# Optimization experiments

Hardware: AMD Instinct MI355X
Metric: run time of the kernel (lower is better)

## Reference

```python
import jax, jax.numpy as jnp
import numpy as np

N_NODES = 100000
N_EDGES = 3200000
IN_DIM, HID1, HID2 = 128, 32, 16


def setup_inputs() -> dict:
    key = jax.random.key(0)
    ks = jax.random.split(key, 4)
    x = jax.random.normal(ks[0], (N_NODES, IN_DIM), dtype=jnp.float32)
    # glorot-ish scaling for weights
    W1 = jax.random.normal(ks[1], (IN_DIM, HID1), dtype=jnp.float32) * (1.0 / np.sqrt(IN_DIM))
    b1 = jnp.zeros((HID1,), dtype=jnp.float32)
    W2 = jax.random.normal(ks[2], (HID1, HID2), dtype=jnp.float32) * (1.0 / np.sqrt(HID1))
    b2 = jnp.zeros((HID2,), dtype=jnp.float32)
    edge_index = jax.random.randint(ks[3], (2, N_EDGES), 0, N_NODES, dtype=jnp.int64)
    return {"x": x, "W1": W1, "b1": b1, "W2": W2, "b2": b2, "edge_index": edge_index}


def _gcn_norm(edge_index, n_nodes):
    # add self loops, then symmetric normalization D^-1/2 (A+I) D^-1/2
    loops = jnp.arange(n_nodes, dtype=edge_index.dtype)
    src = jnp.concatenate([edge_index[0], loops])  # [E+N]
    dst = jnp.concatenate([edge_index[1], loops])
    deg = jax.ops.segment_sum(jnp.ones_like(dst, dtype=jnp.float32), dst, num_segments=n_nodes)
    inv_sqrt = jnp.where(deg > 0, jax.lax.rsqrt(jnp.maximum(deg, 1.0)), 0.0)
    norm = inv_sqrt[src] * inv_sqrt[dst]  # [E+N]
    return src, dst, norm


def _gcn_conv(x, W, b, src, dst, norm, n_nodes):
    xw = x @ W                                   # [N, out] transform first (out < in)
    msg = xw[src] * norm[:, None]                # gather + scale  [E+N, out]
    agg = jax.ops.segment_sum(msg, dst, num_segments=n_nodes)  # scatter-add
    return agg + b


def reference(x, W1, b1, W2, b2, edge_index):
    n = x.shape[0]
    src, dst, norm = _gcn_norm(edge_index, n)  # cached=True: same norm both layers
    h = _gcn_conv(x, W1, b1, src, dst, norm, n)
    h = jax.nn.relu(h)
    out = _gcn_conv(h, W2, b2, src, dst, norm, n)
    return out
```

## Files before the change

### kernel.cpp

```cpp
#include <hip/hip_runtime.h>


#define IN_DIM 128
#define HID1 32
#define HID2 16

#define BSHIFT 8
#define MAXNB 1024
#define SLABCAP 9216
#define P2_TILE 4096
#define P2_PER_THREAD 16

__device__ __forceinline__ float4 f4add(float4 a, float4 b) {
    a.x += b.x; a.y += b.y; a.z += b.z; a.w += b.w; return a;
}

__device__ __forceinline__ void load_edge(const int* __restrict__ e32, int is64,
                                          long e, long E, int& s, int& d) {
    if (is64) { s = e32[2 * e];  d = e32[2 * E + 2 * e]; }
    else      { s = e32[e];      d = e32[E + e]; }
}

__global__ void init_cursors(const int* __restrict__ e32, int* __restrict__ flag,
                             int* __restrict__ bucketCursor, int NB) {
    int i = blockIdx.x * blockDim.x + threadIdx.x;
    if (i < NB) bucketCursor[i] = i * SLABCAP;
    if (blockIdx.x == 0 && threadIdx.x == 0) {
        int is64 = 1;
        for (int k = 0; k < 64; ++k)
            if (e32[2 * k + 1] != 0) { is64 = 0; break; }
        *flag = is64;
    }
}

__global__ __launch_bounds__(256) void partition_edges(const int* __restrict__ e32,
                                                       const int* __restrict__ flag,
                                                       int* __restrict__ bucketCursor,
                                                       unsigned int* __restrict__ part,
                                                       int E, int NB) {
    __shared__ int lbase[MAXNB];
    for (int i = threadIdx.x; i < NB; i += 256) lbase[i] = 0;
    __syncthreads();
    int is64 = *flag;
    long e0 = (long)blockIdx.x * P2_TILE;
    unsigned int v[P2_PER_THREAD];
    int bb[P2_PER_THREAD];
#pragma unroll
    for (int i = 0; i < P2_PER_THREAD; ++i) {
        long e = e0 + threadIdx.x + i * 256;
        if (e < E) {
            int s, d;
            load_edge(e32, is64, e, E, s, d);
            bb[i] = d >> BSHIFT;
            v[i] = (unsigned int)s | ((unsigned int)(d & ((1 << BSHIFT) - 1)) << 17);
            atomicAdd(&lbase[bb[i]], 1);
        } else {
            bb[i] = -1;
        }
    }
    __syncthreads();
    for (int i = threadIdx.x; i < NB; i += 256) {
        int c = lbase[i];
        lbase[i] = c ? atomicAdd(&bucketCursor[i], c) : 0;
    }
    __syncthreads();
#pragma unroll
    for (int i = 0; i < P2_PER_THREAD; ++i) {
        if (bb[i] >= 0) {
            int pos = atomicAdd(&lbase[bb[i]], 1);
            if (pos < (bb[i] + 1) * SLABCAP)
                part[pos] = v[i];
        }
    }
}

__global__ void scan_buckets(const int* __restrict__ bucketCursor,
                             int* __restrict__ bucketStart, int NB) {
    int lane = threadIdx.x;
    int c[16];
    int sum = 0;
#pragma unroll
    for (int k = 0; k < 16; ++k) {
        int idx = lane * 16 + k;
        int sz = 0;
        if (idx < NB) {
            sz = bucketCursor[idx] - idx * SLABCAP;
            if (sz > SLABCAP) sz = SLABCAP;
        }
        c[k] = sz;
        sum += sz;
    }
    int s = sum;
#pragma unroll
    for (int off = 1; off < 64; off <<= 1) {
        int t = __shfl_up(s, off, 64);
        if (lane >= off) s += t;
    }
    int run = s - sum;
#pragma unroll
    for (int k = 0; k < 16; ++k) {
        int idx = lane * 16 + k;
        if (idx < NB) bucketStart[idx] = run;
        run += c[k];
    }
}

__global__ __launch_bounds__(256) void build_rows(const unsigned int* __restrict__ part,
                                                  const int* __restrict__ bucketCursor,
                                                  const int* __restrict__ bucketStart,
                                                  int* __restrict__ rowStart,
                                                  int* __restrict__ cnt,
                                                  float* __restrict__ inv,
                                                  int* __restrict__ srcs, int N) {
    __shared__ unsigned int sSlab[SLABCAP];
    __shared__ int lc[256];
    __shared__ int lofs[256];
    __shared__ int wsum[4];
    int b = blockIdx.x;
    int sbeg = b * SLABCAP;
    int size = bucketCursor[b] - sbeg;
    if (size > SLABCAP) size = SLABCAP;
    int gbase = bucketStart[b];
    int tid = threadIdx.x;
    lc[tid] = 0;
    __syncthreads();
    for (int i = tid; i < size; i += 256) {
        unsigned int v = part[sbeg + i];
        sSlab[i] = v;
        atomicAdd(&lc[v >> 17], 1);
    }
    __syncthreads();
    int c = lc[tid];
    int s = c;
#pragma unroll
    for (int off = 1; off < 64; off <<= 1) {
        int t = __shfl_up(s, off, 64);
        if ((tid & 63) >= off) s += t;
    }
    if ((tid & 63) == 63) wsum[tid >> 6] = s;
    __syncthreads();
    int wb = 0;
    for (int w = 0; w < (tid >> 6); ++w) wb += wsum[w];
    int gstart = gbase + wb + s - c;
    int n = (b << BSHIFT) + tid;
    if (n < N) {
        rowStart[n] = gstart;
        cnt[n] = c;
        inv[n] = rsqrtf((float)(c + 1));
    }
    lofs[tid] = gstart;
    __syncthreads();
    for (int i = tid; i < size; i += 256) {
        unsigned int v = sSlab[i];
        int pos = atomicAdd(&lofs[v >> 17], 1);
        srcs[pos] = (int)(v & 0x1FFFF);
    }
}

__global__ __launch_bounds__(256) void gemm1(const float* __restrict__ x,
                                             const float* __restrict__ W1,
                                             const float* __restrict__ inv,
                                             float* __restrict__ xw, int N) {
    __shared__ float4 sW4[IN_DIM * 8];
    for (int i = threadIdx.x; i < IN_DIM * 8; i += 256)
        sW4[i] = ((const float4*)W1)[i];
    __syncthreads();

    int rq = threadIdx.x >> 3;
    int cq = threadIdx.x & 7;
    int r0 = blockIdx.x * 128 + rq * 4;
    const float4* x4 = (const float4*)x;
    const float4 z4 = make_float4(0.f, 0.f, 0.f, 0.f);

    float4 acc[4];
#pragma unroll
    for (int i = 0; i < 4; ++i) acc[i] = z4;

    for (int k4 = 0; k4 < IN_DIM / 4; ++k4) {
        float4 xa[4];
#pragma unroll
        for (int i = 0; i < 4; ++i) {
            int r = r0 + i;
            xa[i] = (r < N) ? x4[(size_t)r * 32 + k4] : z4;
        }
#pragma unroll
        for (int kk = 0; kk < 4; ++kk) {
            float4 w = sW4[(k4 * 4 + kk) * 8 + cq];
#pragma unroll
            for (int i = 0; i < 4; ++i) {
                float xs = (kk == 0) ? xa[i].x : (kk == 1) ? xa[i].y
                         : (kk == 2) ? xa[i].z : xa[i].w;
                acc[i].x += xs * w.x;
                acc[i].y += xs * w.y;
                acc[i].z += xs * w.z;
                acc[i].w += xs * w.w;
            }
        }
    }

#pragma unroll
    for (int i = 0; i < 4; ++i) {
        int r = r0 + i;
        if (r <= N) {
            float s = (r < N) ? inv[r] : 0.f;
            float4 o;
            o.x = acc[i].x * s; o.y = acc[i].y * s;
            o.z = acc[i].z * s; o.w = acc[i].w * s;
            ((float4*)xw)[(size_t)r * 8 + cq] = o;
        }
    }
}

__global__ __launch_bounds__(256) void agg1_k(const int* __restrict__ rowStart,
                                              const int* __restrict__ cnt,
                                              const int* __restrict__ srcs,
                                              const float* __restrict__ inv,
                                              const float* __restrict__ xw,
                                              const float* __restrict__ b1,
                                              const float* __restrict__ W2,
                                              float* __restrict__ hw, int N) {
    __shared__ float sW2[HID1 * HID2];
    __shared__ float sAgg[4][HID1];
    for (int i = threadIdx.x; i < HID1 * HID2; i += 256) sW2[i] = W2[i];

    int w    = threadIdx.x >> 6;
    int lane = threadIdx.x & 63;
    int node = blockIdx.x * 4 + w;
    int nr   = (node < N) ? node : 0;
    int start = rowStart[nr];
    int len   = (node < N) ? cnt[nr] : 0;
    float invn = (node < N) ? inv[nr] : 0.f;
    int eg = lane >> 3;
    int r  = lane & 7;
    const float4* xw4 = (const float4*)xw;

    float4 acc = make_float4(0.f, 0.f, 0.f, 0.f);
    if (eg == 0) acc = xw4[(size_t)nr * 8 + r];

    int sv = (lane < len) ? srcs[start + lane] : N;
#pragma unroll
    for (int g = 0; g < 8; ++g) {
        int jb = g * 8;
        if (jb < len) {
            int s = __shfl(sv, jb + eg, 64);
            acc = f4add(acc, xw4[(size_t)s * 8 + r]);
        }
    }
    for (int j = 64 + eg; j < len; j += 8)
        acc = f4add(acc, xw4[(size_t)srcs[start + j] * 8 + r]);

#pragma unroll
    for (int off = 32; off >= 8; off >>= 1) {
        acc.x += __shfl_down(acc.x, off, 64);
        acc.y += __shfl_down(acc.y, off, 64);
        acc.z += __shfl_down(acc.z, off, 64);
        acc.w += __shfl_down(acc.w, off, 64);
    }
    if (lane < 8) {
        float4 bb = ((const float4*)b1)[lane];
        float4 o;
        o.x = fmaxf(bb.x + invn * acc.x, 0.f);
        o.y = fmaxf(bb.y + invn * acc.y, 0.f);
        o.z = fmaxf(bb.z + invn * acc.z, 0.f);
        o.w = fmaxf(bb.w + invn * acc.w, 0.f);
        ((float4*)&sAgg[w][0])[lane] = o;
    }
    __syncthreads();

    if (lane < HID2 && node <= N) {
        float y = 0.f;
#pragma unroll
        for (int cc = 0; cc < HID1; ++cc)
            y += sAgg[w][cc] * sW2[cc * HID2 + lane];
        hw[(size_t)node * HID2 + lane] = y * invn;
    }
}

__global__ __launch_bounds__(256) void agg2_k(const int* __restrict__ rowStart,
                                              const int* __restrict__ cnt,
                                              const int* __restrict__ srcs,
                                              const float* __restrict__ inv,
                                              const float* __restrict__ hw,
                                              const float* __restrict__ b2,
                                              float* __restrict__ out, int N) {
    int wave = (blockIdx.x * blockDim.x + threadIdx.x) >> 6;
    int lane = threadIdx.x & 63;
    if (wave >= N) return;
    int n = wave;
    int eg = lane >> 2;
    int q  = lane & 3;
    int start = rowStart[n];
    int len   = cnt[n];
    float invn = inv[n];
    const float4* hw4 = (const float4*)hw;

    float4 acc = make_float4(0.f, 0.f, 0.f, 0.f);
    if (eg == 0) acc = hw4[(size_t)n * 4 + q];

    int sv = (lane < len) ? srcs[start + lane] : N;
#pragma unroll
    for (int g = 0; g < 4; ++g) {
        int jb = g * 16;
        if (jb < len) {
            int s = __shfl(sv, jb + eg, 64);
            acc = f4add(acc, hw4[(size_t)s * 4 + q]);
        }
    }
    for (int j = 64 + eg; j < len; j += 16)
        acc = f4add(acc, hw4[(size_t)srcs[start + j] * 4 + q]);

#pragma unroll
    for (int off = 32; off >= 4; off >>= 1) {
        acc.x += __shfl_down(acc.x, off, 64);
        acc.y += __shfl_down(acc.y, off, 64);
        acc.z += __shfl_down(acc.z, off, 64);
        acc.w += __shfl_down(acc.w, off, 64);
    }
    if (lane < 4) {
        float4 bb = ((const float4*)b2)[lane];
        float4 o;
        o.x = bb.x + invn * acc.x;
        o.y = bb.y + invn * acc.y;
        o.z = bb.z + invn * acc.z;
        o.w = bb.w + invn * acc.w;
        ((float4*)out)[(size_t)n * 4 + lane] = o;
    }
}

extern "C" void kernel_launch(void* const* d_in, const int* in_sizes, int n_in,
                              void* d_out, int out_size, void* d_ws, size_t ws_size,
                              hipStream_t stream) {
    const float* x  = (const float*)d_in[0];
    const float* W1 = (const float*)d_in[1];
    const float* b1 = (const float*)d_in[2];
    const float* W2 = (const float*)d_in[3];
    const float* b2 = (const float*)d_in[4];
    const int*  e32 = (const int*)d_in[5];
    float* out = (float*)d_out;

    const int N = in_sizes[0] / IN_DIM;
    const int E = in_sizes[5] / 2;
    const int Npad = ((N + 63) / 64) * 64;
    const int Epad = ((E + 63) / 64) * 64;
    const int NB   = (N + (1 << BSHIFT) - 1) >> BSHIFT;

    char* ws = (char*)d_ws;
    int*   flag         = (int*)ws;
    int*   bucketCursor = (int*)(ws + 256);
    int*   bucketStart  = bucketCursor + 1088;
    int*   cnt      = bucketStart + 1088;
    int*   rowStart = cnt + Npad;
    float* inv      = (float*)(rowStart + Npad);
    int*   srcs     = (int*)(inv + Npad);
    size_t slab = (size_t)NB * SLABCAP;
    size_t PXW  = slab > (size_t)Npad * HID1 ? slab : (size_t)Npad * HID1;
    unsigned int* part = (unsigned int*)(srcs + Epad);
    float* xw   = (float*)part;
    float* hw   = (float*)(srcs + Epad + PXW);

    init_cursors<<<(NB + 255) / 256, 256, 0, stream>>>(e32, flag, bucketCursor, NB);
    partition_edges<<<(E + P2_TILE - 1) / P2_TILE, 256, 0, stream>>>(
        e32, flag, bucketCursor, part, E, NB);
    scan_buckets<<<1, 64, 0, stream>>>(bucketCursor, bucketStart, NB);
    build_rows<<<NB, 256, 0, stream>>>(part, bucketCursor, bucketStart,
                                       rowStart, cnt, inv, srcs, N);

    gemm1<<<(N + 1 + 127) / 128, 256, 0, stream>>>(x, W1, inv, xw, N);
    agg1_k<<<(N + 1 + 3) / 4, 256, 0, stream>>>(rowStart, cnt, srcs, inv, xw, b1, W2, hw, N);
    agg2_k<<<(N + 3) / 4, 256, 0, stream>>>(rowStart, cnt, srcs, inv, hw, b2, out, N);
}
```

Baseline: 308.0 us.

## Store intermediate features in fp16 and replace bucket scan with atomic offsets

Hidden feature buffers for both layers are written as half precision and converted back to float while accumulating during neighbor gathers. This halves the bytes moved in the gather-heavy aggregation kernels. The separate single-block bucket scan launch is removed; each build_rows block instead claims its global output offset with an atomicAdd on a counter. The trade-offs are lower precision in the intermediate values and bucket placement that depends on block execution order.

```diff
diff --git a/kernel.cpp b/kernel.cpp
--- a/kernel.cpp
+++ b/kernel.cpp
@@ -1,4 +1,5 @@
 #include <hip/hip_runtime.h>
+#include <hip/hip_fp16.h>
 
 
 #define IN_DIM 128
@@ -11,21 +12,25 @@
 #define P2_TILE 4096
 #define P2_PER_THREAD 16
 
-__device__ __forceinline__ float4 f4add(float4 a, float4 b) {
-    a.x += b.x; a.y += b.y; a.z += b.z; a.w += b.w; return a;
-}
-
 __device__ __forceinline__ void load_edge(const int* __restrict__ e32, int is64,
                                           long e, long E, int& s, int& d) {
     if (is64) { s = e32[2 * e];  d = e32[2 * E + 2 * e]; }
     else      { s = e32[e];      d = e32[E + e]; }
 }
 
+__device__ __forceinline__ void h8acc(float4& acc, uint2 u) {
+    __half2 a = *(__half2*)&u.x, b = *(__half2*)&u.y;
+    float2 fa = __half22float2(a), fb = __half22float2(b);
+    acc.x += fa.x; acc.y += fa.y; acc.z += fb.x; acc.w += fb.y;
+}
+
 __global__ void init_cursors(const int* __restrict__ e32, int* __restrict__ flag,
+                             int* __restrict__ total,
                              int* __restrict__ bucketCursor, int NB) {
     int i = blockIdx.x * blockDim.x + threadIdx.x;
     if (i < NB) bucketCursor[i] = i * SLABCAP;
     if (blockIdx.x == 0 && threadIdx.x == 0) {
+        *total = 0;
         int is64 = 1;
         for (int k = 0; k < 64; ++k)
             if (e32[2 * k + 1] != 0) { is64 = 0; break; }
@@ -74,40 +79,9 @@
     }
 }
 
-__global__ void scan_buckets(const int* __restrict__ bucketCursor,
-                             int* __restrict__ bucketStart, int NB) {
-    int lane = threadIdx.x;
-    int c[16];
-    int sum = 0;
-#pragma unroll
-    for (int k = 0; k < 16; ++k) {
-        int idx = lane * 16 + k;
-        int sz = 0;
-        if (idx < NB) {
-            sz = bucketCursor[idx] - idx * SLABCAP;
-            if (sz > SLABCAP) sz = SLABCAP;
-        }
-        c[k] = sz;
-        sum += sz;
-    }
-    int s = sum;
-#pragma unroll
-    for (int off = 1; off < 64; off <<= 1) {
-        int t = __shfl_up(s, off, 64);
-        if (lane >= off) s += t;
-    }
-    int run = s - sum;
-#pragma unroll
-    for (int k = 0; k < 16; ++k) {
-        int idx = lane * 16 + k;
-        if (idx < NB) bucketStart[idx] = run;
-        run += c[k];
-    }
-}
-
 __global__ __launch_bounds__(256) void build_rows(const unsigned int* __restrict__ part,
                                                   const int* __restrict__ bucketCursor,
-                                                  const int* __restrict__ bucketStart,
+                                                  int* __restrict__ total,
                                                   int* __restrict__ rowStart,
                                                   int* __restrict__ cnt,
                                                   float* __restrict__ inv,
@@ -116,11 +90,11 @@
     __shared__ int lc[256];
     __shared__ int lofs[256];
     __shared__ int wsum[4];
+    __shared__ int sGbase;
     int b = blockIdx.x;
     int sbeg = b * SLABCAP;
     int size = bucketCursor[b] - sbeg;
     if (size > SLABCAP) size = SLABCAP;
-    int gbase = bucketStart[b];
     int tid = threadIdx.x;
     lc[tid] = 0;
     __syncthreads();
@@ -129,7 +103,9 @@
         sSlab[i] = v;
         atomicAdd(&lc[v >> 17], 1);
     }
-    __syncthreads();
+    if (tid == 0) sGbase = atomicAdd(total, size);
+    __syncthreads();
+    int gbase = sGbase;
     int c = lc[tid];
     int s = c;
 #pragma unroll
@@ -160,7 +136,7 @@
 __global__ __launch_bounds__(256) void gemm1(const float* __restrict__ x,
                                              const float* __restrict__ W1,
                                              const float* __restrict__ inv,
-                                             float* __restrict__ xw, int N) {
+                                             __half* __restrict__ xwh, int N) {
     __shared__ float4 sW4[IN_DIM * 8];
     for (int i = threadIdx.x; i < IN_DIM * 8; i += 256)
         sW4[i] = ((const float4*)W1)[i];
@@ -202,11 +178,13 @@
     for (int i = 0; i < 4; ++i) {
         int r = r0 + i;
         if (r <= N) {
-            float s = (r < N) ? inv[r] : 0.f;
-            float4 o;
-            o.x = acc[i].x * s; o.y = acc[i].y * s;
-            o.z = acc[i].z * s; o.w = acc[i].w * s;
-            ((float4*)xw)[(size_t)r * 8 + cq] = o;
+            float sc = (r < N) ? inv[r] : 0.f;
+            __half2 p0 = __floats2half2_rn(acc[i].x * sc, acc[i].y * sc);
+            __half2 p1 = __floats2half2_rn(acc[i].z * sc, acc[i].w * sc);
+            uint2 u;
+            u.x = *(unsigned int*)&p0;
+            u.y = *(unsigned int*)&p1;
+            ((uint2*)xwh)[(size_t)r * 8 + cq] = u;
         }
     }
 }
@@ -215,10 +193,10 @@
                                               const int* __restrict__ cnt,
                                               const int* __restrict__ srcs,
                                               const float* __restrict__ inv,
-                                              const float* __restrict__ xw,
+                                              const __half* __restrict__ xwh,
                                               const float* __restrict__ b1,
                                               const float* __restrict__ W2,
-                                              float* __restrict__ hw, int N) {
+                                              __half* __restrict__ hwh, int N) {
     __shared__ float sW2[HID1 * HID2];
     __shared__ float sAgg[4][HID1];
     for (int i = threadIdx.x; i < HID1 * HID2; i += 256) sW2[i] = W2[i];
@@ -232,10 +210,10 @@
     float invn = (node < N) ? inv[nr] : 0.f;
     int eg = lane >> 3;
     int r  = lane & 7;
-    const float4* xw4 = (const float4*)xw;
+    const uint2* xw2 = (const uint2*)xwh;
 
     float4 acc = make_float4(0.f, 0.f, 0.f, 0.f);
-    if (eg == 0) acc = xw4[(size_t)nr * 8 + r];
+    if (eg == 0) h8acc(acc, xw2[(size_t)nr * 8 + r]);
 
     int sv = (lane < len) ? srcs[start + lane] : N;
 #pragma unroll
@@ -243,11 +221,11 @@
         int jb = g * 8;
         if (jb < len) {
             int s = __shfl(sv, jb + eg, 64);
-            acc = f4add(acc, xw4[(size_t)s * 8 + r]);
+            h8acc(acc, xw2[(size_t)s * 8 + r]);
         }
     }
     for (int j = 64 + eg; j < len; j += 8)
-        acc = f4add(acc, xw4[(size_t)srcs[start + j] * 8 + r]);
+        h8acc(acc, xw2[(size_t)srcs[start + j] * 8 + r]);
 
 #pragma unroll
     for (int off = 32; off >= 8; off >>= 1) {
@@ -272,7 +250,7 @@
 #pragma unroll
         for (int cc = 0; cc < HID1; ++cc)
             y += sAgg[w][cc] * sW2[cc * HID2 + lane];
-        hw[(size_t)node * HID2 + lane] = y * invn;
+        hwh[(size_t)node * HID2 + lane] = __float2half_rn(y * invn);
     }
 }
 
@@ -280,7 +258,7 @@
                                               const int* __restrict__ cnt,
                                               const int* __restrict__ srcs,
                                               const float* __restrict__ inv,
-                                              const float* __restrict__ hw,
+                                              const __half* __restrict__ hwh,
                                               const float* __restrict__ b2,
                                               float* __restrict__ out, int N) {
     int wave = (blockIdx.x * blockDim.x + threadIdx.x) >> 6;
@@ -292,10 +270,10 @@
     int start = rowStart[n];
     int len   = cnt[n];
     float invn = inv[n];
-    const float4* hw4 = (const float4*)hw;
+    const uint2* hw2 = (const uint2*)hwh;
 
     float4 acc = make_float4(0.f, 0.f, 0.f, 0.f);
-    if (eg == 0) acc = hw4[(size_t)n * 4 + q];
+    if (eg == 0) h8acc(acc, hw2[(size_t)n * 4 + q]);
 
     int sv = (lane < len) ? srcs[start + lane] : N;
 #pragma unroll
@@ -303,11 +281,11 @@
         int jb = g * 16;
         if (jb < len) {
             int s = __shfl(sv, jb + eg, 64);
-            acc = f4add(acc, hw4[(size_t)s * 4 + q]);
+            h8acc(acc, hw2[(size_t)s * 4 + q]);
         }
     }
     for (int j = 64 + eg; j < len; j += 16)
-        acc = f4add(acc, hw4[(size_t)srcs[start + j] * 4 + q]);
+        h8acc(acc, hw2[(size_t)srcs[start + j] * 4 + q]);
 
 #pragma unroll
     for (int off = 32; off >= 4; off >>= 1) {
@@ -346,26 +324,27 @@
 
     char* ws = (char*)d_ws;
     int*   flag         = (int*)ws;
+    int*   total        = (int*)(ws + 64);
     int*   bucketCursor = (int*)(ws + 256);
-    int*   bucketStart  = bucketCursor + 1088;
-    int*   cnt      = bucketStart + 1088;
+    int*   cnt      = bucketCursor + 1088;
     int*   rowStart = cnt + Npad;
     float* inv      = (float*)(rowStart + Npad);
     int*   srcs     = (int*)(inv + Npad);
-    size_t slab = (size_t)NB * SLABCAP;
-    size_t PXW  = slab > (size_t)Npad * HID1 ? slab : (size_t)Npad * HID1;
+    size_t slabBytes = (size_t)NB * SLABCAP * 4;
     unsigned int* part = (unsigned int*)(srcs + Epad);
-    float* xw   = (float*)part;
-    float* hw   = (float*)(srcs + Epad + PXW);
-
-    init_cursors<<<(NB + 255) / 256, 256, 0, stream>>>(e32, flag, bucketCursor, NB);
+    __half* xwh = (__half*)part;
+    __half* hwh = (__half*)((char*)part + slabBytes);
+
+    init_cursors<<<(NB + 255) / 256, 256, 0, stream>>>(e32, flag, total,
+                                                       bucketCursor, NB);
     partition_edges<<<(E + P2_TILE - 1) / P2_TILE, 256, 0, stream>>>(
         e32, flag, bucketCursor, part, E, NB);
-    scan_buckets<<<1, 64, 0, stream>>>(bucketCursor, bucketStart, NB);
-    build_rows<<<NB, 256, 0, stream>>>(part, bucketCursor, bucketStart,
+    build_rows<<<NB, 256, 0, stream>>>(part, bucketCursor, total,
                                        rowStart, cnt, inv, srcs, N);
 
-    gemm1<<<(N + 1 + 127) / 128, 256, 0, stream>>>(x, W1, inv, xw, N);
-    agg1_k<<<(N + 1 + 3) / 4, 256, 0, stream>>>(rowStart, cnt, srcs, inv, xw, b1, W2, hw, N);
-    agg2_k<<<(N + 3) / 4, 256, 0, stream>>>(rowStart, cnt, srcs, inv, hw, b2, out, N);
-}
+    gemm1<<<(N + 1 + 127) / 128, 256, 0, stream>>>(x, W1, inv, xwh, N);
+    agg1_k<<<(N + 1 + 3) / 4, 256, 0, stream>>>(rowStart, cnt, srcs, inv, xwh,
+                                                b1, W2, hwh, N);
+    agg2_k<<<(N + 3) / 4, 256, 0, stream>>>(rowStart, cnt, srcs, inv, hwh,
+                                            b2, out, N);
+}
```

Result: faster. 299.5 us (-2.8%).
